# Kernel tuning notes

Measured on AMD Instinct MI355X. Metric: run time of the kernel, lower is better.

## Reference

```python
import jax, jax.numpy as jnp
import numpy as np

B, N, F_IN, F_OUT, H, SE_DIM = 16, 1024, 64, 64, 4, 64
ALPHA = 0.2  # LeakyReLU negative slope


def setup_inputs() -> dict:
    key = jax.random.key(0)
    ks = jax.random.split(key, 8)
    x = jax.random.normal(ks[0], (B, N, F_IN), dtype=jnp.float32)
    adj = (jax.random.uniform(ks[1], (B, N, N)) < 0.05).astype(jnp.float32)
    SE = jax.random.normal(ks[2], (N, SE_DIM), dtype=jnp.float32)
    fin = F_IN + SE_DIM
    s_w = float(np.sqrt(2.0) * np.sqrt(6.0 / (fin + F_OUT)))
    s_a = float(np.sqrt(2.0) * np.sqrt(6.0 / (F_OUT + 1)))
    s_p = float(np.sqrt(2.0) * np.sqrt(6.0 / (H + H)))
    W = jax.random.uniform(ks[3], (H, fin, F_OUT), minval=-s_w, maxval=s_w, dtype=jnp.float32)
    a1 = jax.random.uniform(ks[4], (H, F_OUT), minval=-s_a, maxval=s_a, dtype=jnp.float32)
    a2 = jax.random.uniform(ks[5], (H, F_OUT), minval=-s_a, maxval=s_a, dtype=jnp.float32)
    P_l = jax.random.uniform(ks[6], (H, H), minval=-s_p, maxval=s_p, dtype=jnp.float32)
    P_w = jax.random.uniform(ks[7], (H, H), minval=-s_p, maxval=s_p, dtype=jnp.float32)
    return {"x": x, "adj": adj, "SE": SE, "W": W, "a1": a1, "a2": a2, "P_l": P_l, "P_w": P_w}


def reference(x, adj, SE, W, a1, a2, P_l, P_w):
    b, n, _ = x.shape
    # needSE: concat positional/structural embedding (repeated over batch)
    xi = jnp.concatenate([x, jnp.broadcast_to(SE[None], (b, n, SE.shape[-1]))], axis=2)
    # per-head projection: h[b,h,n,o]
    h = jnp.einsum('bnf,hfo->bhno', xi, W)
    f1 = jnp.einsum('bhno,ho->bhn', h, a1)
    f2 = jnp.einsum('bhno,ho->bhn', h, a2)
    # e[b,h,i,j] = leaky_relu(f1[i] + f2[j])
    e = jax.nn.leaky_relu(f1[:, :, :, None] + f2[:, :, None, :], negative_slope=ALPHA)
    # talking-heads mixing before softmax (P_l); softmax over the i (row/source) axis
    e = jnp.einsum('bhij,hg->bgij', e, P_l)
    att = jax.nn.softmax(e, axis=2)
    # talking-heads mixing after softmax (P_w)
    att = jnp.einsum('bgij,gh->bhij', att, P_w)
    # adjacency masking (dropout p=0 -> identity)
    att = att * adj[:, None]
    # aggregation + residual (in == out features, no downsample) + ELU
    out = jnp.einsum('bhij,bhjo->bhio', att, h)
    out = jax.nn.elu(out + x[:, None])
    bb, hh, nn_, oo = out.shape
    # concat heads along feature dim (head order preserved)
    return out.transpose(0, 2, 1, 3).reshape(bb, nn_, hh * oo)
```

## Files before the change

kernel.cpp:

```cpp
#include <hip/hip_runtime.h>
#include <hip/hip_bf16.h>

#define NB 16
#define NN 1024
#define FOUT 64
#define NH 4
#define LRELU_A 0.2f
#define CAP 192

__device__ __forceinline__ float lrelu(float s) { return fmaxf(s, LRELU_A * s); }

__device__ __forceinline__ float4 min4(float4 a, float4 b) {
    return make_float4(fminf(a.x,b.x), fminf(a.y,b.y), fminf(a.z,b.z), fminf(a.w,b.w));
}
__device__ __forceinline__ float4 max4(float4 a, float4 b) {
    return make_float4(fmaxf(a.x,b.x), fmaxf(a.y,b.y), fmaxf(a.z,b.z), fmaxf(a.w,b.w));
}

__global__ __launch_bounds__(256) void k_proj(const float* __restrict__ x,
                                              const float* __restrict__ SE,
                                              const float* __restrict__ W,
                                              const float* __restrict__ a1,
                                              const float* __restrict__ a2,
                                              unsigned int* __restrict__ hb,
                                              float* __restrict__ f1p,
                                              float* __restrict__ f2p)
{
    __shared__ float xi[32 * 128];
    __shared__ float wt[32 * 256];
    const int tid  = threadIdx.x;
    const int row0 = blockIdx.x * 32;
    const int b    = row0 >> 10;
    const int n0   = row0 & 1023;

    const float4* x4  = (const float4*)x;
    const float4* SE4 = (const float4*)SE;
    #pragma unroll
    for (int q = 0; q < 4; ++q) {
        int p  = tid + 256 * q;
        int r  = p >> 5;
        int f4 = p & 31;
        int n  = n0 + r;
        float4 v;
        if (f4 < 16) v = x4[(b * NN + n) * 16 + f4];
        else         v = SE4[n * 16 + (f4 - 16)];
        ((float4*)xi)[p] = v;
    }

    const int tr = tid >> 5;
    const int tc = tid & 31;
    float acc[4][8];
    #pragma unroll
    for (int a_ = 0; a_ < 4; ++a_)
        #pragma unroll
        for (int b_ = 0; b_ < 8; ++b_) acc[a_][b_] = 0.f;

    const float4* W4 = (const float4*)W;
    for (int kk = 0; kk < 4; ++kk) {
        __syncthreads();
        #pragma unroll
        for (int q = 0; q < 8; ++q) {
            int p   = tid + 256 * q;
            int ff  = p >> 6;
            int c4  = p & 63;
            ((float4*)wt)[p] = W4[(c4 >> 4) * 2048 + (kk * 32 + ff) * 16 + (c4 & 15)];
        }
        __syncthreads();
        #pragma unroll
        for (int f4i = 0; f4i < 8; ++f4i) {
            float4 xv[4];
            #pragma unroll
            for (int rr = 0; rr < 4; ++rr)
                xv[rr] = ((const float4*)xi)[(tr + 8 * rr) * 32 + kk * 8 + f4i];
            #pragma unroll
            for (int c = 0; c < 4; ++c) {
                const int ffl = f4i * 4 + c;
                float2 wv[4];
                #pragma unroll
                for (int hp = 0; hp < 4; ++hp)
                    wv[hp] = ((const float2*)wt)[ffl * 128 + 32 * hp + tc];
                #pragma unroll
                for (int rr = 0; rr < 4; ++rr) {
                    float xc = (c == 0) ? xv[rr].x : (c == 1) ? xv[rr].y
                             : (c == 2) ? xv[rr].z : xv[rr].w;
                    #pragma unroll
                    for (int hp = 0; hp < 4; ++hp) {
                        acc[rr][2*hp]   = fmaf(xc, wv[hp].x, acc[rr][2*hp]);
                        acc[rr][2*hp+1] = fmaf(xc, wv[hp].y, acc[rr][2*hp+1]);
                    }
                }
            }
        }
    }

    float av1[8], av2[8];
    #pragma unroll
    for (int k = 0; k < 8; ++k) {
        int hp = k >> 1;
        int o  = tc * 2 + (k & 1);
        av1[k] = a1[hp * 64 + o];
        av2[k] = a2[hp * 64 + o];
    }

    #pragma unroll
    for (int rr = 0; rr < 4; ++rr) {
        int n = n0 + tr + 8 * rr;
        #pragma unroll
        for (int hp = 0; hp < 4; ++hp) {
            union { struct { __hip_bfloat16 x, y; } v; unsigned int u; } pk;
            pk.v.x = __float2bfloat16(acc[rr][2*hp]);
            pk.v.y = __float2bfloat16(acc[rr][2*hp+1]);
            hb[((size_t)(b * NH + hp) * NN + n) * 32 + tc] = pk.u;
        }
    }

    #pragma unroll
    for (int rr = 0; rr < 4; ++rr) {
        #pragma unroll
        for (int hp = 0; hp < 4; ++hp) {
            float s1 = fmaf(acc[rr][2*hp], av1[2*hp], acc[rr][2*hp+1] * av1[2*hp+1]);
            float s2 = fmaf(acc[rr][2*hp], av2[2*hp], acc[rr][2*hp+1] * av2[2*hp+1]);
            #pragma unroll
            for (int mseg = 16; mseg > 0; mseg >>= 1) {
                s1 += __shfl_xor(s1, mseg);
                s2 += __shfl_xor(s2, mseg);
            }
            if (tc == 0) {
                int n = n0 + tr + 8 * rr;
                f1p[(b * NN + n) * 4 + hp] = s1;
                f2p[(b * NN + n) * 4 + hp] = s2;
            }
        }
    }
}

__global__ __launch_bounds__(256) void k_stats(const float* __restrict__ f1p,
                                               const float* __restrict__ f2p,
                                               const float* __restrict__ P_l,
                                               float* __restrict__ Mp,
                                               float* __restrict__ Rp)
{
    __shared__ float4 f1s[1024];
    __shared__ float4 mns[256];
    __shared__ float4 mxs[256];
    __shared__ float4 red[8][32];
    const int tid = threadIdx.x;
    const int b   = blockIdx.x >> 5;
    const int jt  = blockIdx.x & 31;
    const float4* f1p4 = (const float4*)f1p;
    const float4* f2p4 = (const float4*)f2p;

    float4 mn = make_float4( INFINITY,  INFINITY,  INFINITY,  INFINITY);
    float4 mx = make_float4(-INFINITY, -INFINITY, -INFINITY, -INFINITY);
    #pragma unroll
    for (int q = 0; q < 4; ++q) {
        float4 v = f1p4[b * NN + tid + 256 * q];
        f1s[tid + 256 * q] = v;
        mn = min4(mn, v);
        mx = max4(mx, v);
    }
    mns[tid] = mn; mxs[tid] = mx;
    __syncthreads();
    for (int s = 128; s > 0; s >>= 1) {
        if (tid < s) {
            mns[tid] = min4(mns[tid], mns[tid + s]);
            mxs[tid] = max4(mxs[tid], mxs[tid + s]);
        }
        __syncthreads();
    }
    mn = mns[0]; mx = mxs[0];

    float pl[4][4];
    #pragma unroll
    for (int hh = 0; hh < 4; ++hh)
        #pragma unroll
        for (int g = 0; g < 4; ++g) pl[hh][g] = P_l[hh * 4 + g];

    const int jj = tid & 31, ic = tid >> 5;
    const int j  = jt * 32 + jj;
    float4 f2v = f2p4[b * NN + j];
    float f2a[4] = {f2v.x, f2v.y, f2v.z, f2v.w};
    float mna[4] = {mn.x, mn.y, mn.z, mn.w};
    float mxa[4] = {mx.x, mx.y, mx.z, mx.w};
    float mub[4];
    #pragma unroll
    for (int g = 0; g < 4; ++g) {
        float s = 0.f;
        #pragma unroll
        for (int hh = 0; hh < 4; ++hh) {
            float base = (pl[hh][g] >= 0.f ? mxa[hh] : mna[hh]) + f2a[hh];
            s = fmaf(pl[hh][g], lrelu(base), s);
        }
        mub[g] = s;
    }

    float d[4] = {0.f, 0.f, 0.f, 0.f};
    const int i0 = ic * 128;
    #pragma unroll 2
    for (int i = i0; i < i0 + 128; ++i) {
        float4 f1v = f1s[i];
        float l0 = lrelu(f1v.x + f2a[0]);
        float l1 = lrelu(f1v.y + f2a[1]);
        float l2 = lrelu(f1v.z + f2a[2]);
        float l3 = lrelu(f1v.w + f2a[3]);
        #pragma unroll
        for (int g = 0; g < 4; ++g) {
            float e = fmaf(pl[0][g], l0, fmaf(pl[1][g], l1, fmaf(pl[2][g], l2, pl[3][g] * l3)));
            d[g] += __expf(e - mub[g]);
        }
    }
    red[ic][jj] = make_float4(d[0], d[1], d[2], d[3]);
    __syncthreads();
    if (ic == 0) {
        float4 t = red[0][jj];
        #pragma unroll
        for (int r = 1; r < 8; ++r) {
            float4 u = red[r][jj];
            t.x += u.x; t.y += u.y; t.z += u.z; t.w += u.w;
        }
        ((float4*)Rp)[b * NN + j] = make_float4(1.f / t.x, 1.f / t.y, 1.f / t.z, 1.f / t.w);
        ((float4*)Mp)[b * NN + j] = make_float4(mub[0], mub[1], mub[2], mub[3]);
    }
}

__global__ __launch_bounds__(256) void k_agg(const float* __restrict__ adj,
                                             const float* __restrict__ x,
                                             const unsigned int* __restrict__ hb,
                                             const float* __restrict__ f1p,
                                             const float* __restrict__ f2p,
                                             const float* __restrict__ Mp,
                                             const float* __restrict__ Rp,
                                             const float* __restrict__ P_l,
                                             const float* __restrict__ P_w,
                                             float* __restrict__ out)
{
    __shared__ int   jl[4][CAP];
    __shared__ float attl[4][CAP * 4 + 4];
    const int tid  = threadIdx.x;
    const int w    = tid >> 6;
    const int lane = tid & 63;
    const int row  = blockIdx.x * 4 + w;
    const int b    = row >> 10;

    const float4* arow = (const float4*)adj + (size_t)row * 256;
    float4 av[4];
    #pragma unroll
    for (int q = 0; q < 4; ++q) av[q] = arow[lane + 64 * q];

    const unsigned long long lt = (1ull << lane) - 1ull;
    int cnt = 0;
    #pragma unroll
    for (int q = 0; q < 4; ++q) {
        float vv[4] = {av[q].x, av[q].y, av[q].z, av[q].w};
        #pragma unroll
        for (int c = 0; c < 4; ++c) {
            bool nz = (vv[c] != 0.f);
            unsigned long long mask = __ballot(nz);
            if (nz) {
                int pos = cnt + __popcll(mask & lt);
                if (pos < CAP) jl[w][pos] = (lane + 64 * q) * 4 + c;
            }
            cnt += __popcll(mask);
        }
    }
    if (cnt > CAP) cnt = CAP;
    __syncthreads();

    float pl[4][4], pw[4][4];
    #pragma unroll
    for (int a_ = 0; a_ < 4; ++a_)
        #pragma unroll
        for (int g = 0; g < 4; ++g) {
            pl[a_][g] = P_l[a_ * 4 + g];
            pw[a_][g] = P_w[a_ * 4 + g];
        }
    const float4 f1v = ((const float4*)f1p)[row];
    for (int base = 0; base < cnt; base += 64) {
        int kk = base + lane;
        if (kk < cnt) {
            int j = jl[w][kk];
            float4 f2v = ((const float4*)f2p)[b * NN + j];
            float4 mv  = ((const float4*)Mp)[b * NN + j];
            float4 rv  = ((const float4*)Rp)[b * NN + j];
            float l0 = lrelu(f1v.x + f2v.x);
            float l1 = lrelu(f1v.y + f2v.y);
            float l2 = lrelu(f1v.z + f2v.z);
            float l3 = lrelu(f1v.w + f2v.w);
            float p0 = __expf(fmaf(pl[0][0], l0, fmaf(pl[1][0], l1, fmaf(pl[2][0], l2, pl[3][0] * l3))) - mv.x) * rv.x;
            float p1 = __expf(fmaf(pl[0][1], l0, fmaf(pl[1][1], l1, fmaf(pl[2][1], l2, pl[3][1] * l3))) - mv.y) * rv.y;
            float p2 = __expf(fmaf(pl[0][2], l0, fmaf(pl[1][2], l1, fmaf(pl[2][2], l2, pl[3][2] * l3))) - mv.z) * rv.z;
            float p3 = __expf(fmaf(pl[0][3], l0, fmaf(pl[1][3], l1, fmaf(pl[2][3], l2, pl[3][3] * l3))) - mv.w) * rv.w;
            float at0 = fmaf(p0, pw[0][0], fmaf(p1, pw[1][0], fmaf(p2, pw[2][0], p3 * pw[3][0])));
            float at1 = fmaf(p0, pw[0][1], fmaf(p1, pw[1][1], fmaf(p2, pw[2][1], p3 * pw[3][1])));
            float at2 = fmaf(p0, pw[0][2], fmaf(p1, pw[1][2], fmaf(p2, pw[2][2], p3 * pw[3][2])));
            float at3 = fmaf(p0, pw[0][3], fmaf(p1, pw[1][3], fmaf(p2, pw[2][3], p3 * pw[3][3])));
            ((float4*)&attl[w][0])[kk] = make_float4(at0, at1, at2, at3);
        }
    }
    __syncthreads();

    const int hh = lane >> 4;
    const int og = lane & 15;
    const uint2* hrow = (const uint2*)hb + ((size_t)(b * NH + hh) * NN) * 16 + og;
    float a0 = 0.f, a1_ = 0.f, a2_ = 0.f, a3_ = 0.f;
    #pragma unroll 4
    for (int kk = 0; kk < cnt; ++kk) {
        int   j  = jl[w][kk];
        float at = attl[w][kk * 4 + hh];
        uint2 u  = hrow[(size_t)j * 16];
        a0 = fmaf(at, __uint_as_float(u.x << 16),         a0);
        a1_ = fmaf(at, __uint_as_float(u.x & 0xffff0000u), a1_);
        a2_ = fmaf(at, __uint_as_float(u.y << 16),         a2_);
        a3_ = fmaf(at, __uint_as_float(u.y & 0xffff0000u), a3_);
    }
    float4 xr = ((const float4*)x)[row * 16 + og];
    float r0 = a0  + xr.x;
    float r1 = a1_ + xr.y;
    float r2 = a2_ + xr.z;
    float r3 = a3_ + xr.w;
    float4 o4;
    o4.x = (r0 > 0.f) ? r0 : (__expf(r0) - 1.f);
    o4.y = (r1 > 0.f) ? r1 : (__expf(r1) - 1.f);
    o4.z = (r2 > 0.f) ? r2 : (__expf(r2) - 1.f);
    o4.w = (r3 > 0.f) ? r3 : (__expf(r3) - 1.f);
    ((float4*)out)[(size_t)row * 64 + hh * 16 + og] = o4;
}

extern "C" void kernel_launch(void* const* d_in, const int* in_sizes, int n_in,
                              void* d_out, int out_size, void* d_ws, size_t ws_size,
                              hipStream_t stream)
{
    (void)in_sizes; (void)n_in; (void)out_size; (void)ws_size;
    const float* x   = (const float*)d_in[0];
    const float* adj = (const float*)d_in[1];
    const float* SE  = (const float*)d_in[2];
    const float* W   = (const float*)d_in[3];
    const float* a1  = (const float*)d_in[4];
    const float* a2  = (const float*)d_in[5];
    const float* P_l = (const float*)d_in[6];
    const float* P_w = (const float*)d_in[7];
    float* out = (float*)d_out;

    float* f1p = (float*)d_ws;
    float* f2p = f1p + 65536;
    float* Mp  = f2p + 65536;
    float* Rp  = Mp  + 65536;
    unsigned int* hbu = (unsigned int*)(Rp + 65536);

    k_proj <<<512,  256, 0, stream>>>(x, SE, W, a1, a2, hbu, f1p, f2p);
    k_stats<<<512,  256, 0, stream>>>(f1p, f2p, P_l, Mp, Rp);
    k_agg  <<<4096, 256, 0, stream>>>(adj, x, hbu, f1p, f2p, Mp, Rp, P_l, P_w, out);
}
```

Measured before the change: 186.5 us.

## Use bf16 MFMA for projection, split f1/f2 kernel, batch gather loads in aggregation

Rewrites the projection as a bf16 MFMA GEMM. A new prep kernel transposes and swizzles W to bf16, and a separate kernel computes f1/f2 from the stored bf16 h. The stats kernel's shared-memory tree reduction becomes wave shuffles. The aggregation kernel stores attention transposed, pads the neighbor list, and issues 8 gathers per iteration for more memory-level parallelism. Barriers within a wave are replaced by lgkmcnt waits. The changes add two extra kernel launches, and f1/f2 are now computed from bf16-rounded h, which shifts precision slightly.

```diff
diff --git a/kernel.cpp b/kernel.cpp
--- a/kernel.cpp
+++ b/kernel.cpp
@@ -8,6 +8,11 @@
 #define LRELU_A 0.2f
 #define CAP 192
 
+typedef __attribute__((ext_vector_type(8))) short bf16x8;
+typedef __attribute__((ext_vector_type(4))) float f32x4;
+
+#define WFENCE() asm volatile("s_waitcnt lgkmcnt(0)" ::: "memory")
+
 __device__ __forceinline__ float lrelu(float s) { return fmaxf(s, LRELU_A * s); }
 
 __device__ __forceinline__ float4 min4(float4 a, float4 b) {
@@ -17,119 +22,131 @@
     return make_float4(fmaxf(a.x,b.x), fmaxf(a.y,b.y), fmaxf(a.z,b.z), fmaxf(a.w,b.w));
 }
 
+__device__ __forceinline__ unsigned int pk2(float a, float b) {
+    union { __hip_bfloat16 h; unsigned short u; } ua, ub;
+    ua.h = __float2bfloat16(a); ub.h = __float2bfloat16(b);
+    return (unsigned int)ua.u | ((unsigned int)ub.u << 16);
+}
+__device__ __forceinline__ unsigned short bfbits(float a) {
+    union { __hip_bfloat16 h; unsigned short u; } ua;
+    ua.h = __float2bfloat16(a);
+    return ua.u;
+}
+__device__ __forceinline__ int toff(int r, int c) { return (r * 16 + (c ^ (r & 7))) * 16; }
+
+__global__ __launch_bounds__(256) void k_prep(const float* __restrict__ W,
+                                              uint4* __restrict__ WbT)
+{
+    int gid  = blockIdx.x * 256 + threadIdx.x;
+    int col  = gid >> 4, c = gid & 15;
+    int head = col >> 6, o = col & 63;
+    const float* wp = W + head * 8192 + (c * 8) * 64 + o;
+    float v[8];
+    #pragma unroll
+    for (int j = 0; j < 8; ++j) v[j] = wp[j * 64];
+    uint4 outv = { pk2(v[0], v[1]), pk2(v[2], v[3]), pk2(v[4], v[5]), pk2(v[6], v[7]) };
+    WbT[col * 16 + (c ^ (col & 7))] = outv;
+}
+
 __global__ __launch_bounds__(256) void k_proj(const float* __restrict__ x,
                                               const float* __restrict__ SE,
-                                              const float* __restrict__ W,
-                                              const float* __restrict__ a1,
-                                              const float* __restrict__ a2,
-                                              unsigned int* __restrict__ hb,
-                                              float* __restrict__ f1p,
-                                              float* __restrict__ f2p)
-{
-    __shared__ float xi[32 * 128];
-    __shared__ float wt[32 * 256];
-    const int tid  = threadIdx.x;
-    const int row0 = blockIdx.x * 32;
-    const int b    = row0 >> 10;
-    const int n0   = row0 & 1023;
-
-    const float4* x4  = (const float4*)x;
-    const float4* SE4 = (const float4*)SE;
-    #pragma unroll
-    for (int q = 0; q < 4; ++q) {
-        int p  = tid + 256 * q;
-        int r  = p >> 5;
-        int f4 = p & 31;
-        int n  = n0 + r;
-        float4 v;
-        if (f4 < 16) v = x4[(b * NN + n) * 16 + f4];
-        else         v = SE4[n * 16 + (f4 - 16)];
-        ((float4*)xi)[p] = v;
-    }
-
-    const int tr = tid >> 5;
-    const int tc = tid & 31;
-    float acc[4][8];
-    #pragma unroll
-    for (int a_ = 0; a_ < 4; ++a_)
-        #pragma unroll
-        for (int b_ = 0; b_ < 8; ++b_) acc[a_][b_] = 0.f;
-
-    const float4* W4 = (const float4*)W;
-    for (int kk = 0; kk < 4; ++kk) {
-        __syncthreads();
+                                              const uint4* __restrict__ WbT,
+                                              unsigned int* __restrict__ hbu)
+{
+    __shared__ char smem[49152];
+    char* Ab = smem;
+    char* Bb = smem + 32768;
+    const int tid = threadIdx.x;
+    const int rt  = blockIdx.x >> 2;
+    const int ch  = blockIdx.x & 3;
+
+    {
+        const int row = tid & 127, kh = tid >> 7;
+        const int rg = rt * 128 + row;
+        const int bb = rg >> 10, nn = rg & 1023;
+        const float4* src = (kh == 0) ? (const float4*)(x + ((size_t)(bb * NN + nn)) * 64)
+                                      : (const float4*)(SE + (size_t)nn * 64);
         #pragma unroll
         for (int q = 0; q < 8; ++q) {
-            int p   = tid + 256 * q;
-            int ff  = p >> 6;
-            int c4  = p & 63;
-            ((float4*)wt)[p] = W4[(c4 >> 4) * 2048 + (kk * 32 + ff) * 16 + (c4 & 15)];
-        }
-        __syncthreads();
-        #pragma unroll
-        for (int f4i = 0; f4i < 8; ++f4i) {
-            float4 xv[4];
+            float4 u0 = src[q * 2], u1 = src[q * 2 + 1];
+            uint4 pkv = { pk2(u0.x, u0.y), pk2(u0.z, u0.w), pk2(u1.x, u1.y), pk2(u1.z, u1.w) };
+            *(uint4*)(Ab + toff(row, kh * 8 + q)) = pkv;
+        }
+    }
+    {
+        const uint4* wsrc = WbT + ch * 1024;
+        #pragma unroll
+        for (int q = 0; q < 4; ++q) ((uint4*)Bb)[tid + 256 * q] = wsrc[tid + 256 * q];
+    }
+    __syncthreads();
+
+    const int l = tid & 63, w = tid >> 6;
+    const int r0 = 32 * w + (l & 15);
+    const int ci = l >> 4;
+    f32x4 acc[2][4];
+    #pragma unroll
+    for (int a = 0; a < 2; ++a)
+        #pragma unroll
+        for (int bf = 0; bf < 4; ++bf) { acc[a][bf][0]=0.f; acc[a][bf][1]=0.f; acc[a][bf][2]=0.f; acc[a][bf][3]=0.f; }
+
+    #pragma unroll
+    for (int ks = 0; ks < 4; ++ks) {
+        const int c = 4 * ks + ci;
+        bf16x8 A0 = *(const bf16x8*)(Ab + toff(r0,      c));
+        bf16x8 A1 = *(const bf16x8*)(Ab + toff(r0 + 16, c));
+        #pragma unroll
+        for (int bf = 0; bf < 4; ++bf) {
+            bf16x8 Bf = *(const bf16x8*)(Bb + toff(16 * bf + (l & 15), c));
+            acc[0][bf] = __builtin_amdgcn_mfma_f32_16x16x32_bf16(A0, Bf, acc[0][bf], 0, 0, 0);
+            acc[1][bf] = __builtin_amdgcn_mfma_f32_16x16x32_bf16(A1, Bf, acc[1][bf], 0, 0, 0);
+        }
+    }
+    __syncthreads();
+
+    unsigned short* cst = (unsigned short*)smem + w * 2048;
+    #pragma unroll
+    for (int a = 0; a < 2; ++a)
+        #pragma unroll
+        for (int bf = 0; bf < 4; ++bf)
             #pragma unroll
-            for (int rr = 0; rr < 4; ++rr)
-                xv[rr] = ((const float4*)xi)[(tr + 8 * rr) * 32 + kk * 8 + f4i];
-            #pragma unroll
-            for (int c = 0; c < 4; ++c) {
-                const int ffl = f4i * 4 + c;
-                float2 wv[4];
-                #pragma unroll
-                for (int hp = 0; hp < 4; ++hp)
-                    wv[hp] = ((const float2*)wt)[ffl * 128 + 32 * hp + tc];
-                #pragma unroll
-                for (int rr = 0; rr < 4; ++rr) {
-                    float xc = (c == 0) ? xv[rr].x : (c == 1) ? xv[rr].y
-                             : (c == 2) ? xv[rr].z : xv[rr].w;
-                    #pragma unroll
-                    for (int hp = 0; hp < 4; ++hp) {
-                        acc[rr][2*hp]   = fmaf(xc, wv[hp].x, acc[rr][2*hp]);
-                        acc[rr][2*hp+1] = fmaf(xc, wv[hp].y, acc[rr][2*hp+1]);
-                    }
-                }
+            for (int reg = 0; reg < 4; ++reg) {
+                int r   = 16 * a + (l >> 4) * 4 + reg;
+                int col = 16 * bf + (l & 15);
+                cst[r * 64 + col] = bfbits(acc[a][bf][reg]);
             }
-        }
-    }
-
-    float av1[8], av2[8];
-    #pragma unroll
-    for (int k = 0; k < 8; ++k) {
-        int hp = k >> 1;
-        int o  = tc * 2 + (k & 1);
-        av1[k] = a1[hp * 64 + o];
-        av2[k] = a2[hp * 64 + o];
-    }
-
-    #pragma unroll
-    for (int rr = 0; rr < 4; ++rr) {
-        int n = n0 + tr + 8 * rr;
-        #pragma unroll
-        for (int hp = 0; hp < 4; ++hp) {
-            union { struct { __hip_bfloat16 x, y; } v; unsigned int u; } pk;
-            pk.v.x = __float2bfloat16(acc[rr][2*hp]);
-            pk.v.y = __float2bfloat16(acc[rr][2*hp+1]);
-            hb[((size_t)(b * NH + hp) * NN + n) * 32 + tc] = pk.u;
-        }
-    }
-
-    #pragma unroll
-    for (int rr = 0; rr < 4; ++rr) {
-        #pragma unroll
-        for (int hp = 0; hp < 4; ++hp) {
-            float s1 = fmaf(acc[rr][2*hp], av1[2*hp], acc[rr][2*hp+1] * av1[2*hp+1]);
-            float s2 = fmaf(acc[rr][2*hp], av2[2*hp], acc[rr][2*hp+1] * av2[2*hp+1]);
-            #pragma unroll
-            for (int mseg = 16; mseg > 0; mseg >>= 1) {
-                s1 += __shfl_xor(s1, mseg);
-                s2 += __shfl_xor(s2, mseg);
-            }
-            if (tc == 0) {
-                int n = n0 + tr + 8 * rr;
-                f1p[(b * NN + n) * 4 + hp] = s1;
-                f2p[(b * NN + n) * 4 + hp] = s2;
-            }
+    WFENCE();
+    const uint4* csv = (const uint4*)cst;
+    #pragma unroll
+    for (int p = 0; p < 4; ++p) {
+        int idx = p * 64 + l;
+        uint4 v = csv[idx];
+        int r = idx >> 3, o8 = idx & 7;
+        int ng = rt * 128 + 32 * w + r;
+        int bb = ng >> 10, n2 = ng & 1023;
+        ((uint4*)hbu)[((size_t)(bb * NH + ch) * NN + n2) * 8 + o8] = v;
+    }
+}
+
+__global__ __launch_bounds__(256) void k_f12(const unsigned short* __restrict__ hb,
+                                             const float* __restrict__ a1,
+                                             const float* __restrict__ a2,
+                                             float* __restrict__ f1p,
+                                             float* __restrict__ f2p)
+{
+    int task = blockIdx.x * 4 + (threadIdx.x >> 6);
+    int lane = threadIdx.x & 63;
+    int b = task >> 10, n = task & 1023;
+    #pragma unroll
+    for (int hh = 0; hh < NH; ++hh) {
+        unsigned short us = hb[((size_t)(b * NH + hh) * NN + n) * 64 + lane];
+        float v  = __uint_as_float((unsigned int)us << 16);
+        float s1 = v * a1[hh * 64 + lane];
+        float s2 = v * a2[hh * 64 + lane];
+        #pragma unroll
+        for (int m = 32; m > 0; m >>= 1) { s1 += __shfl_xor(s1, m); s2 += __shfl_xor(s2, m); }
+        if (lane == 0) {
+            f1p[(b * NN + n) * 4 + hh] = s1;
+            f2p[(b * NN + n) * 4 + hh] = s2;
         }
     }
 }
@@ -141,34 +158,33 @@
                                                float* __restrict__ Rp)
 {
     __shared__ float4 f1s[1024];
-    __shared__ float4 mns[256];
-    __shared__ float4 mxs[256];
     __shared__ float4 red[8][32];
-    const int tid = threadIdx.x;
+    const int tid  = threadIdx.x;
+    const int lane = tid & 63;
     const int b   = blockIdx.x >> 5;
     const int jt  = blockIdx.x & 31;
     const float4* f1p4 = (const float4*)f1p;
     const float4* f2p4 = (const float4*)f2p;
 
+    #pragma unroll
+    for (int q = 0; q < 4; ++q) f1s[tid + 256 * q] = f1p4[b * NN + tid + 256 * q];
+    __syncthreads();
+
     float4 mn = make_float4( INFINITY,  INFINITY,  INFINITY,  INFINITY);
     float4 mx = make_float4(-INFINITY, -INFINITY, -INFINITY, -INFINITY);
     #pragma unroll
-    for (int q = 0; q < 4; ++q) {
-        float4 v = f1p4[b * NN + tid + 256 * q];
-        f1s[tid + 256 * q] = v;
+    for (int q = 0; q < 16; ++q) {
+        float4 v = f1s[lane + 64 * q];
         mn = min4(mn, v);
         mx = max4(mx, v);
     }
-    mns[tid] = mn; mxs[tid] = mx;
-    __syncthreads();
-    for (int s = 128; s > 0; s >>= 1) {
-        if (tid < s) {
-            mns[tid] = min4(mns[tid], mns[tid + s]);
-            mxs[tid] = max4(mxs[tid], mxs[tid + s]);
-        }
-        __syncthreads();
-    }
-    mn = mns[0]; mx = mxs[0];
+    #pragma unroll
+    for (int m = 32; m > 0; m >>= 1) {
+        float4 on = make_float4(__shfl_xor(mn.x, m), __shfl_xor(mn.y, m), __shfl_xor(mn.z, m), __shfl_xor(mn.w, m));
+        float4 ox = make_float4(__shfl_xor(mx.x, m), __shfl_xor(mx.y, m), __shfl_xor(mx.z, m), __shfl_xor(mx.w, m));
+        mn = min4(mn, on);
+        mx = max4(mx, ox);
+    }
 
     float pl[4][4];
     #pragma unroll
@@ -234,8 +250,8 @@
                                              const float* __restrict__ P_w,
                                              float* __restrict__ out)
 {
-    __shared__ int   jl[4][CAP];
-    __shared__ float attl[4][CAP * 4 + 4];
+    __shared__ int   jl[4][CAP + 8];
+    __shared__ float attlT[4][4][CAP + 8];
     const int tid  = threadIdx.x;
     const int w    = tid >> 6;
     const int lane = tid & 63;
@@ -264,7 +280,7 @@
         }
     }
     if (cnt > CAP) cnt = CAP;
-    __syncthreads();
+    WFENCE();
 
     float pl[4][4], pw[4][4];
     #pragma unroll
@@ -290,28 +306,70 @@
             float p1 = __expf(fmaf(pl[0][1], l0, fmaf(pl[1][1], l1, fmaf(pl[2][1], l2, pl[3][1] * l3))) - mv.y) * rv.y;
             float p2 = __expf(fmaf(pl[0][2], l0, fmaf(pl[1][2], l1, fmaf(pl[2][2], l2, pl[3][2] * l3))) - mv.z) * rv.z;
             float p3 = __expf(fmaf(pl[0][3], l0, fmaf(pl[1][3], l1, fmaf(pl[2][3], l2, pl[3][3] * l3))) - mv.w) * rv.w;
-            float at0 = fmaf(p0, pw[0][0], fmaf(p1, pw[1][0], fmaf(p2, pw[2][0], p3 * pw[3][0])));
-            float at1 = fmaf(p0, pw[0][1], fmaf(p1, pw[1][1], fmaf(p2, pw[2][1], p3 * pw[3][1])));
-            float at2 = fmaf(p0, pw[0][2], fmaf(p1, pw[1][2], fmaf(p2, pw[2][2], p3 * pw[3][2])));
-            float at3 = fmaf(p0, pw[0][3], fmaf(p1, pw[1][3], fmaf(p2, pw[2][3], p3 * pw[3][3])));
-            ((float4*)&attl[w][0])[kk] = make_float4(at0, at1, at2, at3);
-        }
-    }
-    __syncthreads();
+            #pragma unroll
+            for (int g = 0; g < 4; ++g)
+                attlT[w][g][kk] =
+                    fmaf(p0, pw[0][g], fmaf(p1, pw[1][g], fmaf(p2, pw[2][g], p3 * pw[3][g])));
+        }
+    }
+    if (lane < 8) {
+        jl[w][cnt + lane] = 0;
+        #pragma unroll
+        for (int g = 0; g < 4; ++g) attlT[w][g][cnt + lane] = 0.f;
+    }
+    WFENCE();
 
     const int hh = lane >> 4;
     const int og = lane & 15;
     const uint2* hrow = (const uint2*)hb + ((size_t)(b * NH + hh) * NN) * 16 + og;
+    const float* atp = &attlT[w][hh][0];
     float a0 = 0.f, a1_ = 0.f, a2_ = 0.f, a3_ = 0.f;
-    #pragma unroll 4
-    for (int kk = 0; kk < cnt; ++kk) {
-        int   j  = jl[w][kk];
-        float at = attl[w][kk * 4 + hh];
-        uint2 u  = hrow[(size_t)j * 16];
-        a0 = fmaf(at, __uint_as_float(u.x << 16),         a0);
-        a1_ = fmaf(at, __uint_as_float(u.x & 0xffff0000u), a1_);
-        a2_ = fmaf(at, __uint_as_float(u.y << 16),         a2_);
-        a3_ = fmaf(at, __uint_as_float(u.y & 0xffff0000u), a3_);
+    #pragma unroll 1
+    for (int base = 0; base < cnt; base += 8) {
+        const int4   ja = *(const int4*)&jl[w][base];
+        const int4   jb = *(const int4*)&jl[w][base + 4];
+        const float4 ta = *(const float4*)&atp[base];
+        const float4 tb = *(const float4*)&atp[base + 4];
+        uint2 u0 = hrow[(size_t)ja.x * 16];
+        uint2 u1 = hrow[(size_t)ja.y * 16];
+        uint2 u2 = hrow[(size_t)ja.z * 16];
+        uint2 u3 = hrow[(size_t)ja.w * 16];
+        uint2 u4 = hrow[(size_t)jb.x * 16];
+        uint2 u5 = hrow[(size_t)jb.y * 16];
+        uint2 u6 = hrow[(size_t)jb.z * 16];
+        uint2 u7 = hrow[(size_t)jb.w * 16];
+        a0 = fmaf(ta.x, __uint_as_float(u0.x << 16), a0);
+        a1_ = fmaf(ta.x, __uint_as_float(u0.x & 0xffff0000u), a1_);
+        a2_ = fmaf(ta.x, __uint_as_float(u0.y << 16), a2_);
+        a3_ = fmaf(ta.x, __uint_as_float(u0.y & 0xffff0000u), a3_);
+        a0 = fmaf(ta.y, __uint_as_float(u1.x << 16), a0);
+        a1_ = fmaf(ta.y, __uint_as_float(u1.x & 0xffff0000u), a1_);
+        a2_ = fmaf(ta.y, __uint_as_float(u1.y << 16), a2_);
+        a3_ = fmaf(ta.y, __uint_as_float(u1.y & 0xffff0000u), a3_);
+        a0 = fmaf(ta.z, __uint_as_float(u2.x << 16), a0);
+        a1_ = fmaf(ta.z, __uint_as_float(u2.x & 0xffff0000u), a1_);
+        a2_ = fmaf(ta.z, __uint_as_float(u2.y << 16), a2_);
+        a3_ = fmaf(ta.z, __uint_as_float(u2.y & 0xffff0000u), a3_);
+        a0 = fmaf(ta.w, __uint_as_float(u3.x << 16), a0);
+        a1_ = fmaf(ta.w, __uint_as_float(u3.x & 0xffff0000u), a1_);
+        a2_ = fmaf(ta.w, __uint_as_float(u3.y << 16), a2_);
+        a3_ = fmaf(ta.w, __uint_as_float(u3.y & 0xffff0000u), a3_);
+        a0 = fmaf(tb.x, __uint_as_float(u4.x << 16), a0);
+        a1_ = fmaf(tb.x, __uint_as_float(u4.x & 0xffff0000u), a1_);
+        a2_ = fmaf(tb.x, __uint_as_float(u4.y << 16), a2_);
+        a3_ = fmaf(tb.x, __uint_as_float(u4.y & 0xffff0000u), a3_);
+        a0 = fmaf(tb.y, __uint_as_float(u5.x << 16), a0);
+        a1_ = fmaf(tb.y, __uint_as_float(u5.x & 0xffff0000u), a1_);
+        a2_ = fmaf(tb.y, __uint_as_float(u5.y << 16), a2_);
+        a3_ = fmaf(tb.y, __uint_as_float(u5.y & 0xffff0000u), a3_);
+        a0 = fmaf(tb.z, __uint_as_float(u6.x << 16), a0);
+        a1_ = fmaf(tb.z, __uint_as_float(u6.x & 0xffff0000u), a1_);
+        a2_ = fmaf(tb.z, __uint_as_float(u6.y << 16), a2_);
+        a3_ = fmaf(tb.z, __uint_as_float(u6.y & 0xffff0000u), a3_);
+        a0 = fmaf(tb.w, __uint_as_float(u7.x << 16), a0);
+        a1_ = fmaf(tb.w, __uint_as_float(u7.x & 0xffff0000u), a1_);
+        a2_ = fmaf(tb.w, __uint_as_float(u7.y << 16), a2_);
+        a3_ = fmaf(tb.w, __uint_as_float(u7.y & 0xffff0000u), a3_);
     }
     float4 xr = ((const float4*)x)[row * 16 + og];
     float r0 = a0  + xr.x;
@@ -346,8 +404,11 @@
     float* Mp  = f2p + 65536;
     float* Rp  = Mp  + 65536;
     unsigned int* hbu = (unsigned int*)(Rp + 65536);
-
-    k_proj <<<512,  256, 0, stream>>>(x, SE, W, a1, a2, hbu, f1p, f2p);
+    uint4* WbT = (uint4*)(hbu + 2097152);
+
+    k_prep <<<16,   256, 0, stream>>>(W, WbT);
+    k_proj <<<512,  256, 0, stream>>>(x, SE, WbT, hbu);
+    k_f12  <<<4096, 256, 0, stream>>>((const unsigned short*)hbu, a1, a2, f1p, f2p);
     k_stats<<<512,  256, 0, stream>>>(f1p, f2p, P_l, Mp, Rp);
     k_agg  <<<4096, 256, 0, stream>>>(adj, x, hbu, f1p, f2p, Mp, Rp, P_l, P_w, out);
 }
```

Measured after the change: 189.6 us. No clear change (+1.7%).
